# Kernel optimization log

Hardware: AMD Instinct MI355X
Metric: run time of the kernel (lower is better)

## Reference

```python
import jax, jax.numpy as jnp
import numpy as np

B, T_IN, T_OUT, N, C, H, K1 = 4, 12, 24, 5000, 32, 8, 17  # K1 = k+1 (self included)
SIGMA_RATIO = 2.0
BETA = 0.8  # Swish beta
W_THRESH = 1e-5


def setup_inputs() -> dict:
    key = jax.random.key(0)
    k1, k2, k3, k4, k5 = jax.random.split(key, 5)
    x = jax.random.normal(k1, (B, T_IN, N, C), jnp.float32)
    nearest_nodes = jax.random.randint(k2, (N, K1), 0, N)  # int indices; -1 allowed by module semantics
    nearest_dists = jax.random.uniform(k3, (N, K1), jnp.float32) * 100.0
    W_shrink = jax.random.normal(k4, (T_IN * H, T_OUT - T_IN), jnp.float32) / np.float32(np.sqrt(T_IN * H))
    b_shrink = jax.random.normal(k5, (T_OUT - T_IN,), jnp.float32) * 0.01
    return {"x": x, "nearest_nodes": nearest_nodes, "nearest_dists": nearest_dists,
            "W_shrink": W_shrink, "b_shrink": b_shrink}


def reference(x, nearest_nodes, nearest_dists, W_shrink, b_shrink):
    Bx, t, n, c = x.shape
    sigma = nearest_dists.max() / SIGMA_RATIO
    lam = jnp.arange(1, H + 1, dtype=jnp.float32) / H  # (H,)
    nd = nearest_dists.reshape(-1)                      # (N*K1,)
    nn = nearest_nodes.reshape(-1)                      # (N*K1,)
    # GCN weights: exp(-d^2 * lambda / sigma^2), zeroed for missing (-1) neighbors and tiny values
    w = jnp.exp(-(nd[:, None] ** 2) * lam / (sigma ** 2))  # (N*K1, H)
    w = jnp.where(nn[:, None] == -1, 0.0, w)
    w = jnp.where(w < W_THRESH, 0.0, w)
    # pad row so index -1 hits zeros (jax -1 wraps to last row, matching torch)
    pad_x = jnp.concatenate([x, jnp.zeros((Bx, t, 1, c), x.dtype)], axis=2)
    x_nb = pad_x[:, :, nn].reshape(Bx, t, n, K1, c)         # gathered neighbors (B,t,N,K1,C)
    w3 = w.reshape(n, K1, H)
    # fused gather-weight-sum over neighbor dim j -> (B,t,N,H,C)
    agg = jnp.einsum('btnjc,njh->btnhc', x_nb, w3)
    # (B,t,N,H,C) -> (B,N,C,t,H) -> (B,N,C,t*H)
    feat = agg.transpose(0, 2, 4, 1, 3).reshape(Bx, n, c, t * H)
    y = feat @ W_shrink + b_shrink                          # (B,N,C,T-t_in)
    y = y.transpose(0, 3, 1, 2)                             # (B,T-t_in,N,C)
    y = y * jax.nn.sigmoid(BETA * y)                        # Swish
    return jnp.concatenate([x, y], axis=1)                  # (B,T,N,C)
```

## Files before the change

kernel.cpp:

```cpp
#include <hip/hip_runtime.h>

#define BB     4
#define T_IN   12
#define T_OUT  24
#define NNODES 5000
#define CC     32
#define HH     8
#define K1     17
#define O_OUT  12
#define XSTRIDE (NNODES*CC)
#define TPU     (NNODES*16)

#define XB2_BN  192
#define XB2_B   (NNODES*XB2_BN)
#define JP      9
#define VJPD    36
#define VQD     (JP*VJPD)
#define VND     (4*VQD)
#define WJN     144

__global__ void max_reduce_kernel(const float* __restrict__ d, int n,
                                  unsigned* __restrict__ out) {
    float m = 0.0f;
    for (int i = blockIdx.x * blockDim.x + threadIdx.x; i < n;
         i += gridDim.x * blockDim.x)
        m = fmaxf(m, d[i]);
#pragma unroll
    for (int off = 32; off > 0; off >>= 1)
        m = fmaxf(m, __shfl_down(m, off, 64));
    if ((threadIdx.x & 63) == 0)
        atomicMax(out, __float_as_uint(m));
}

__device__ inline unsigned bf16rne(float f) {
    unsigned u = __float_as_uint(f);
    return (u + 0x7FFFu + ((u >> 16) & 1u)) >> 16;
}

__global__ void prep4_kernel(const float4* __restrict__ x,
                             float4* __restrict__ out,
                             uint4* __restrict__ xb2,
                             const int* __restrict__ nn,
                             const float* __restrict__ nd,
                             const unsigned* __restrict__ maxbits,
                             float* __restrict__ wjg) {
    const int gs = gridDim.x * blockDim.x;
    const int g0 = blockIdx.x * blockDim.x + threadIdx.x;

    const int totalA = BB * T_IN * NNODES;
    for (int i = g0; i < totalA; i += gs) {
        int bt = i / NNODES;
        int nd_ = i - bt * NNODES;
        int b  = bt / T_IN;
        int t  = bt - b * T_IN;
        const float4* xr = x + (size_t)i * 8;
        float4* orow = out + ((size_t)(b * T_OUT + t) * NNODES + nd_) * 8;
        uint4* xrow  = xb2 + ((size_t)(b * NNODES + nd_) * T_IN + t) * 4;
#pragma unroll
        for (int vq = 0; vq < 4; ++vq) {
            float4 v0 = xr[2 * vq], v1 = xr[2 * vq + 1];
            orow[2 * vq] = v0; orow[2 * vq + 1] = v1;
            uint4 pk;
            pk.x = bf16rne(v0.x) | (bf16rne(v0.y) << 16);
            pk.y = bf16rne(v0.z) | (bf16rne(v0.w) << 16);
            pk.z = bf16rne(v1.x) | (bf16rne(v1.y) << 16);
            pk.w = bf16rne(v1.z) | (bf16rne(v1.w) << 16);
            xrow[vq] = pk;
        }
    }

    float mx = __uint_as_float(*maxbits);
    float inv_s2 = 4.0f / (mx * mx);
    const int totalB = NNODES * WJN;
    for (int i = g0; i < totalB; i += gs) {
        int n = i / WJN;
        int r = i - n * WJN;
        int j = r >> 3, h = r & 7;
        float wv = 0.f;
        if (j < K1) {
            float dv = nd[n * K1 + j];
            float lam = (float)(h + 1) * 0.125f;
            wv = expf(-dv * dv * lam * inv_s2);
            if (nn[n * K1 + j] == -1 || wv < 1e-5f) wv = 0.0f;
        }
        wjg[i] = wv;
    }
}

struct VBlk { uint4 v[9]; };

__device__ __forceinline__ unsigned u4c(const uint4& u, int i) {
    switch (i) { case 0: return u.x; case 1: return u.y;
                 case 2: return u.z; default: return u.w; }
}

#define DOT2(ACC, XP, VP) \
    asm("v_dot2_f32_bf16 %0, %1, %2, %0" : "+v"(ACC) : "v"(XP), "v"(VP))

__launch_bounds__(256)
__global__ void gnn_main7_kernel(const unsigned* __restrict__ xb2,
                                 const float* __restrict__ wjg,
                                 const float* __restrict__ Wsh,
                                 const int* __restrict__ nn,
                                 const float* __restrict__ bsh,
                                 float* __restrict__ out) {
    __shared__ float pb2[2][24][65];
    __shared__ unsigned Vl[VND];
    __shared__ float bl[O_OUT];

    const int n    = blockIdx.x;
    const int tid  = threadIdx.x;
    const int q    = __builtin_amdgcn_readfirstlane(tid >> 6);
    const int lane = tid & 63;
    const int bb   = lane >> 4;
    const int c2   = lane & 15;

    if (tid < O_OUT) bl[tid] = bsh[tid];

    int nnv[18];
#pragma unroll
    for (int j = 0; j < K1; ++j) nnv[j] = max(nn[n * K1 + j], 0);
    nnv[17] = nnv[16];

    const unsigned* xlane = xb2 + bb * XB2_B + 48 * q + c2;

#define XLOADP(E0, E1, E2, O0, O1, O2, JPI) do {                             \
        const unsigned* xe_ = xlane + nnv[2 * (JPI)] * XB2_BN;               \
        const unsigned* xo_ = xlane + nnv[2 * (JPI) + 1] * XB2_BN;           \
        E0 = xe_[0]; E1 = xe_[16]; E2 = xe_[32];                             \
        O0 = xo_[0]; O1 = xo_[16]; O2 = xo_[32];                             \
    } while (0)

    unsigned e00, e01, e02, o00, o01, o02;
    unsigned e10, e11, e12, o10, o11, o12;
    unsigned e20, e21, e22, o20, o21, o22;

    XLOADP(e00, e01, e02, o00, o01, o02, 0);
    XLOADP(e10, e11, e12, o10, o11, o12, 1);

    {
        const int t = tid / 12;
        const int o = tid - t * 12;
        float Wcol[8];
        if (tid < 144) {
#pragma unroll
            for (int h = 0; h < 8; ++h) Wcol[h] = Wsh[(t * 8 + h) * 12 + o];
        }
        const float* wp = wjg + n * WJN;
        const int vi = (t / 3) * VQD + (t % 3) * 12 + o;
#pragma unroll
        for (int jp = 0; jp < JP; ++jp) {
            float wa[16];
#pragma unroll
            for (int h = 0; h < 16; ++h) wa[h] = wp[jp * 16 + h];
            if (tid < 144) {
                float v0 = 0.f, v1 = 0.f;
#pragma unroll
                for (int h = 0; h < 8; ++h) {
                    v0 = fmaf(wa[h],     Wcol[h], v0);
                    v1 = fmaf(wa[8 + h], Wcol[h], v1);
                }
                Vl[vi + jp * VJPD] = bf16rne(v0) | (bf16rne(v1) << 16);
            }
        }
    }

    float pf[24];
#pragma unroll
    for (int i = 0; i < 24; ++i) pf[i] = 0.f;

    __syncthreads();

#define VLOADP(DST, JPI) do {                                                \
        const uint4* vp_ = (const uint4*)&Vl[q * VQD + (JPI) * VJPD];        \
        _Pragma("unroll")                                                    \
        for (int i_ = 0; i_ < 9; ++i_) DST.v[i_] = vp_[i_];                  \
    } while (0)

#define COMPP(VV, E0, E1, E2, O0, O1, O2) do {                               \
        unsigned xe_[3] = {E0, E1, E2};                                      \
        unsigned xo_[3] = {O0, O1, O2};                                      \
        _Pragma("unroll")                                                    \
        for (int t_ = 0; t_ < 3; ++t_) {                                     \
            unsigned plo_ = __builtin_amdgcn_perm(xe_[t_], xo_[t_],          \
                                                  0x01000504u);              \
            unsigned phi_ = __builtin_amdgcn_perm(xe_[t_], xo_[t_],          \
                                                  0x03020706u);              \
            _Pragma("unroll")                                                \
            for (int o_ = 0; o_ < 12; ++o_) {                                \
                unsigned vp_ = u4c(VV.v[t_ * 3 + (o_ >> 2)], o_ & 3);        \
                DOT2(pf[o_],      plo_, vp_);                                \
                DOT2(pf[12 + o_], phi_, vp_);                                \
            }                                                                \
        }                                                                    \
    } while (0)

    VBlk va, vb;
    VLOADP(va, 0);
    VLOADP(vb, 1);
    XLOADP(e20, e21, e22, o20, o21, o22, 2);
    COMPP(va, e00, e01, e02, o00, o01, o02);
    VLOADP(va, 2);
    XLOADP(e00, e01, e02, o00, o01, o02, 3);
    COMPP(vb, e10, e11, e12, o10, o11, o12);
    VLOADP(vb, 3);
    XLOADP(e10, e11, e12, o10, o11, o12, 4);
    COMPP(va, e20, e21, e22, o20, o21, o22);
    VLOADP(va, 4);
    XLOADP(e20, e21, e22, o20, o21, o22, 5);
    COMPP(vb, e00, e01, e02, o00, o01, o02);
    VLOADP(vb, 5);
    XLOADP(e00, e01, e02, o00, o01, o02, 6);
    COMPP(va, e10, e11, e12, o10, o11, o12);
    VLOADP(va, 6);
    XLOADP(e10, e11, e12, o10, o11, o12, 7);
    COMPP(vb, e20, e21, e22, o20, o21, o22);
    VLOADP(vb, 7);
    XLOADP(e20, e21, e22, o20, o21, o22, 8);
    COMPP(va, e00, e01, e02, o00, o01, o02);
    VLOADP(va, 8);
    COMPP(vb, e10, e11, e12, o10, o11, o12);
    COMPP(va, e20, e21, e22, o20, o21, o22);

#undef VLOADP
#undef XLOADP
#undef COMPP

    if (q >= 2) {
#pragma unroll
        for (int i = 0; i < 24; ++i) pb2[q - 2][i][lane] = pf[i];
    }
    __syncthreads();
    if (q < 2) {
#pragma unroll
        for (int i = 0; i < 24; ++i) pf[i] += pb2[q][i][lane];
    }
    if (q == 1) {
#pragma unroll
        for (int i = 0; i < 24; ++i) pb2[1][i][lane] = pf[i];
    }
    __syncthreads();
    if (q == 0) {
        float* ob = out + ((size_t)(bb * T_OUT + T_IN) * NNODES + n) * CC + 2 * c2;
#pragma unroll
        for (int o = 0; o < O_OUT; ++o) {
            float v0 = pf[o]      + pb2[1][o][lane]      + bl[o];
            float v1 = pf[12 + o] + pb2[1][12 + o][lane] + bl[o];
            float s0 = v0 / (1.f + expf(-0.8f * v0));
            float s1 = v1 / (1.f + expf(-0.8f * v1));
            *(float2*)(ob + (size_t)o * XSTRIDE) = make_float2(s0, s1);
        }
    }
}

template <int PACK>
__global__ void prep_kernel(const float4* __restrict__ x,
                            float4* __restrict__ out,
                            uint2* __restrict__ xb) {
    const int PLANE4 = NNODES * CC / 4;
    const int total  = BB * T_IN * PLANE4;
    for (int i = blockIdx.x * blockDim.x + threadIdx.x; i < total;
         i += gridDim.x * blockDim.x) {
        int bt = i / PLANE4;
        int qq = i - bt * PLANE4;
        int b  = bt / T_IN;
        int t  = bt - b * T_IN;
        float4 v = x[i];
        out[((size_t)(b * T_OUT + t)) * PLANE4 + qq] = v;
        if (PACK) {
            uint2 pk;
            pk.x = bf16rne(v.x) | (bf16rne(v.y) << 16);
            pk.y = bf16rne(v.z) | (bf16rne(v.w) << 16);
            xb[i] = pk;
        }
    }
}

template <int USEBF>
__launch_bounds__(256)
__global__ void gnn_main_kernel(const float* __restrict__ x,
                                const unsigned* __restrict__ xbu,
                                const int* __restrict__ nn,
                                const float* __restrict__ nd,
                                const float* __restrict__ Wsh,
                                const float* __restrict__ bsh,
                                const unsigned* __restrict__ maxbits,
                                float* __restrict__ out) {
    __shared__ float wl[K1][HH];
    __shared__ float Wl[96][O_OUT];
    __shared__ float bl_s[O_OUT];
    __shared__ int   nnl[K1];

    const int n   = blockIdx.x;
    const int tid = threadIdx.x;
    const int rg  = tid >> 4;
    const int c2  = tid & 15;
    const int b   = rg >> 2;
    const int q   = rg & 3;

    for (int i = tid; i < 288; i += 256)
        ((float4*)Wl)[i] = ((const float4*)Wsh)[i];
    if (tid < O_OUT) bl_s[tid] = bsh[tid];
    if (tid < K1 * HH) {
        int j = tid >> 3, h = tid & 7;
        int v = nn[n * K1 + j];
        float dv = nd[n * K1 + j];
        float mx = __uint_as_float(*maxbits);
        float inv_s2 = 4.0f / (mx * mx);
        float lam = (float)(h + 1) * 0.125f;
        float wv = expf(-dv * dv * lam * inv_s2);
        if (v == -1 || wv < 1e-5f) wv = 0.0f;
        wl[j][h] = wv;
    }
    if (tid < K1) nnl[tid] = max(nn[n * K1 + tid], 0);
    __syncthreads();

    float acc[3][2][8];
#pragma unroll
    for (int k = 0; k < 3; ++k)
#pragma unroll
        for (int cc = 0; cc < 2; ++cc)
#pragma unroll
            for (int h = 0; h < 8; ++h) acc[k][cc][h] = 0.f;

    if (USEBF) {
        const unsigned* xbase = xbu + (b * T_IN + 3 * q) * TPU + c2;
        unsigned ua0, ua1, ua2, ub0, ub1, ub2;
#define LOADB(u0, u1, u2, J) do {                                            \
        int idx_ = __builtin_amdgcn_readfirstlane(nnl[(J)]);                 \
        const unsigned* bp_ = xbase + idx_ * 16;                             \
        u0 = bp_[0]; u1 = bp_[TPU]; u2 = bp_[2 * TPU];                       \
    } while (0)
#define COMPB(u0, u1, u2, J) do {                                            \
        float4 wA_ = *(const float4*)&wl[(J)][0];                            \
        float4 wB_ = *(const float4*)&wl[(J)][4];                            \
        float wv_[8] = {wA_.x, wA_.y, wA_.z, wA_.w,                          \
                        wB_.x, wB_.y, wB_.z, wB_.w};                         \
        float xl_[3] = {__uint_as_float(u0 << 16),                           \
                        __uint_as_float(u1 << 16),                           \
                        __uint_as_float(u2 << 16)};                          \
        float xh_[3] = {__uint_as_float(u0 & 0xffff0000u),                   \
                        __uint_as_float(u1 & 0xffff0000u),                   \
                        __uint_as_float(u2 & 0xffff0000u)};                  \
        _Pragma("unroll")                                                    \
        for (int k_ = 0; k_ < 3; ++k_)                                       \
            _Pragma("unroll")                                                \
            for (int h_ = 0; h_ < 8; ++h_) {                                 \
                acc[k_][0][h_] = fmaf(wv_[h_], xl_[k_], acc[k_][0][h_]);     \
                acc[k_][1][h_] = fmaf(wv_[h_], xh_[k_], acc[k_][1][h_]);     \
            }                                                                \
    } while (0)
        LOADB(ua0, ua1, ua2, 0);
#pragma unroll 1
        for (int jj = 0; jj < 8; ++jj) {
            LOADB(ub0, ub1, ub2, 2 * jj + 1);
            COMPB(ua0, ua1, ua2, 2 * jj);
            LOADB(ua0, ua1, ua2, 2 * jj + 2);
            COMPB(ub0, ub1, ub2, 2 * jj + 1);
        }
        COMPB(ua0, ua1, ua2, 16);
#undef LOADB
#undef COMPB
    } else {
        const float* xbase = x + (b * T_IN + 3 * q) * XSTRIDE + 2 * c2;
        float2 xa0, xa1, xa2, xb0, xb1, xb2;
#define LOADJ(v0, v1, v2, J) do {                                            \
        int idx_ = __builtin_amdgcn_readfirstlane(nnl[(J)]);                 \
        const float* bp_ = xbase + idx_ * CC;                                \
        v0 = *(const float2*)(bp_);                                          \
        v1 = *(const float2*)(bp_ + XSTRIDE);                                \
        v2 = *(const float2*)(bp_ + 2 * XSTRIDE);                            \
    } while (0)
#define COMPJ(v0, v1, v2, J) do {                                            \
        float4 wA_ = *(const float4*)&wl[(J)][0];                            \
        float4 wB_ = *(const float4*)&wl[(J)][4];                            \
        float wv_[8] = {wA_.x, wA_.y, wA_.z, wA_.w,                          \
                        wB_.x, wB_.y, wB_.z, wB_.w};                         \
        float xv_[3][2] = {{v0.x, v0.y}, {v1.x, v1.y}, {v2.x, v2.y}};        \
        _Pragma("unroll")                                                    \
        for (int k_ = 0; k_ < 3; ++k_)                                       \
            _Pragma("unroll")                                                \
            for (int cc_ = 0; cc_ < 2; ++cc_)                                \
                _Pragma("unroll")                                            \
                for (int h_ = 0; h_ < 8; ++h_)                               \
                    acc[k_][cc_][h_] =                                       \
                        fmaf(wv_[h_], xv_[k_][cc_], acc[k_][cc_][h_]);       \
    } while (0)
        LOADJ(xa0, xa1, xa2, 0);
#pragma unroll 1
        for (int jj = 0; jj < 8; ++jj) {
            LOADJ(xb0, xb1, xb2, 2 * jj + 1);
            COMPJ(xa0, xa1, xa2, 2 * jj);
            LOADJ(xa0, xa1, xa2, 2 * jj + 2);
            COMPJ(xb0, xb1, xb2, 2 * jj + 1);
        }
        COMPJ(xa0, xa1, xa2, 16);
#undef LOADJ
#undef COMPJ
    }

    float p[2][O_OUT];
#pragma unroll
    for (int o = 0; o < O_OUT; ++o) { p[0][o] = 0.f; p[1][o] = 0.f; }
#pragma unroll
    for (int k = 0; k < 3; ++k) {
#pragma unroll
        for (int h = 0; h < 8; ++h) {
            int row = (3 * q + k) * 8 + h;
            const float4* wr = (const float4*)&Wl[row][0];
            float4 w0 = wr[0], w1 = wr[1], w2 = wr[2];
            float wrow[12] = {w0.x, w0.y, w0.z, w0.w,
                              w1.x, w1.y, w1.z, w1.w,
                              w2.x, w2.y, w2.z, w2.w};
            float a0 = acc[k][0][h], a1 = acc[k][1][h];
#pragma unroll
            for (int o = 0; o < O_OUT; ++o) {
                p[0][o] = fmaf(a0, wrow[o], p[0][o]);
                p[1][o] = fmaf(a1, wrow[o], p[1][o]);
            }
        }
    }
#pragma unroll
    for (int cc = 0; cc < 2; ++cc)
#pragma unroll
        for (int o = 0; o < O_OUT; ++o) {
            float v = p[cc][o];
            v += __shfl_xor(v, 16, 64);
            v += __shfl_xor(v, 32, 64);
            p[cc][o] = v;
        }
    if (q == 0) {
        float* ob = out + ((size_t)(b * T_OUT + T_IN) * NNODES + n) * CC + 2 * c2;
#pragma unroll
        for (int o = 0; o < O_OUT; ++o) {
            float v0 = p[0][o] + bl_s[o];
            float v1 = p[1][o] + bl_s[o];
            float s0 = v0 / (1.f + expf(-0.8f * v0));
            float s1 = v1 / (1.f + expf(-0.8f * v1));
            *(float2*)(ob + (size_t)o * XSTRIDE) = make_float2(s0, s1);
        }
    }
}

extern "C" void kernel_launch(void* const* d_in, const int* in_sizes, int n_in,
                              void* d_out, int out_size, void* d_ws, size_t ws_size,
                              hipStream_t stream) {
    const float* x   = (const float*)d_in[0];
    const int*   nn  = (const int*)d_in[1];
    const float* nd  = (const float*)d_in[2];
    const float* Wsh = (const float*)d_in[3];
    const float* bsh = (const float*)d_in[4];
    float* out = (float*)d_out;

    unsigned* maxbits = (unsigned*)d_ws;
    hipMemsetAsync(d_ws, 0, sizeof(unsigned), stream);
    max_reduce_kernel<<<128, 256, 0, stream>>>(nd, NNODES * K1, maxbits);

    const size_t wjg_off = 1024;
    const size_t wjg_sz  = (size_t)NNODES * WJN * 4;
    const size_t xb2_off = wjg_off + wjg_sz;
    const size_t xb2_sz  = (size_t)BB * NNODES * T_IN * 16 * 4;
    const size_t need2   = xb2_off + xb2_sz;

    if (ws_size >= need2) {
        float* wjg = (float*)((char*)d_ws + wjg_off);
        uint4* xb2 = (uint4*)((char*)d_ws + xb2_off);

        prep4_kernel<<<2048, 256, 0, stream>>>(
            (const float4*)x, (float4*)out, xb2, nn, nd, maxbits, wjg);
        gnn_main7_kernel<<<NNODES, 256, 0, stream>>>(
            (const unsigned*)xb2, wjg, Wsh, nn, bsh, out);
    } else {
        unsigned* xbu = (unsigned*)((char*)d_ws + 256);
        const size_t need1 = 256 + (size_t)BB * T_IN * NNODES * CC * 2;
        if (ws_size >= need1) {
            prep_kernel<1><<<2048, 256, 0, stream>>>((const float4*)x,
                                                     (float4*)out, (uint2*)xbu);
            gnn_main_kernel<1><<<NNODES, 256, 0, stream>>>(x, xbu, nn, nd, Wsh,
                                                           bsh, maxbits, out);
        } else {
            prep_kernel<0><<<2048, 256, 0, stream>>>((const float4*)x,
                                                     (float4*)out, (uint2*)xbu);
            gnn_main_kernel<0><<<NNODES, 256, 0, stream>>>(x, xbu, nn, nd, Wsh,
                                                           bsh, maxbits, out);
        }
    }
}
```

Measured before the change: 86.42 us.

## Fold max-reduce into prep kernel and compute GCN weights inside main kernel

Drops the separate max-reduction launch by having the prep kernel compute the distance max with an atomic. The per-node Gaussian weights are no longer written to a global workspace buffer. Each main-kernel block now computes its 144 weights in shared memory before building its bf16 V table. This saves one kernel launch and a global write/read of the weight table, at the cost of an extra block barrier and exp work inside the main kernel.

Measured after the change: 90.61 us. 1.05x slower.

```diff
diff --git a/kernel.cpp b/kernel.cpp
--- a/kernel.cpp
+++ b/kernel.cpp
@@ -17,7 +17,6 @@
 #define VJPD    36
 #define VQD     (JP*VJPD)
 #define VND     (4*VQD)
-#define WJN     144
 
 __global__ void max_reduce_kernel(const float* __restrict__ d, int n,
                                   unsigned* __restrict__ out) {
@@ -37,15 +36,23 @@
     return (u + 0x7FFFu + ((u >> 16) & 1u)) >> 16;
 }
 
-__global__ void prep4_kernel(const float4* __restrict__ x,
+__global__ void prep5_kernel(const float4* __restrict__ x,
                              float4* __restrict__ out,
                              uint4* __restrict__ xb2,
-                             const int* __restrict__ nn,
                              const float* __restrict__ nd,
-                             const unsigned* __restrict__ maxbits,
-                             float* __restrict__ wjg) {
+                             unsigned* __restrict__ maxbits) {
     const int gs = gridDim.x * blockDim.x;
     const int g0 = blockIdx.x * blockDim.x + threadIdx.x;
+
+    {
+        float m = 0.0f;
+        for (int i = g0; i < NNODES * K1; i += gs) m = fmaxf(m, nd[i]);
+#pragma unroll
+        for (int off = 32; off > 0; off >>= 1)
+            m = fmaxf(m, __shfl_down(m, off, 64));
+        if ((threadIdx.x & 63) == 0 && m > 0.0f)
+            atomicMax(maxbits, __float_as_uint(m));
+    }
 
     const int totalA = BB * T_IN * NNODES;
     for (int i = g0; i < totalA; i += gs) {
@@ -68,23 +75,6 @@
             xrow[vq] = pk;
         }
     }
-
-    float mx = __uint_as_float(*maxbits);
-    float inv_s2 = 4.0f / (mx * mx);
-    const int totalB = NNODES * WJN;
-    for (int i = g0; i < totalB; i += gs) {
-        int n = i / WJN;
-        int r = i - n * WJN;
-        int j = r >> 3, h = r & 7;
-        float wv = 0.f;
-        if (j < K1) {
-            float dv = nd[n * K1 + j];
-            float lam = (float)(h + 1) * 0.125f;
-            wv = expf(-dv * dv * lam * inv_s2);
-            if (nn[n * K1 + j] == -1 || wv < 1e-5f) wv = 0.0f;
-        }
-        wjg[i] = wv;
-    }
 }
 
 struct VBlk { uint4 v[9]; };
@@ -98,14 +88,16 @@
     asm("v_dot2_f32_bf16 %0, %1, %2, %0" : "+v"(ACC) : "v"(XP), "v"(VP))
 
 __launch_bounds__(256)
-__global__ void gnn_main7_kernel(const unsigned* __restrict__ xb2,
-                                 const float* __restrict__ wjg,
+__global__ void gnn_main9_kernel(const unsigned* __restrict__ xb2,
+                                 const float* __restrict__ nd,
                                  const float* __restrict__ Wsh,
                                  const int* __restrict__ nn,
                                  const float* __restrict__ bsh,
+                                 const unsigned* __restrict__ maxbits,
                                  float* __restrict__ out) {
     __shared__ float pb2[2][24][65];
     __shared__ unsigned Vl[VND];
+    __shared__ float wjl[144];
     __shared__ float bl[O_OUT];
 
     const int n    = blockIdx.x;
@@ -138,30 +130,43 @@
     XLOADP(e00, e01, e02, o00, o01, o02, 0);
     XLOADP(e10, e11, e12, o10, o11, o12, 1);
 
-    {
-        const int t = tid / 12;
-        const int o = tid - t * 12;
-        float Wcol[8];
-        if (tid < 144) {
-#pragma unroll
-            for (int h = 0; h < 8; ++h) Wcol[h] = Wsh[(t * 8 + h) * 12 + o];
-        }
-        const float* wp = wjg + n * WJN;
-        const int vi = (t / 3) * VQD + (t % 3) * 12 + o;
+    const int t14 = tid / 12;
+    const int o14 = tid - t14 * 12;
+    float Wcol[8];
+    if (tid < 144) {
+#pragma unroll
+        for (int h = 0; h < 8; ++h) Wcol[h] = Wsh[(t14 * 8 + h) * 12 + o14];
+        int j = tid >> 3, h = tid & 7;
+        float wv = 0.f;
+        if (j < K1) {
+            float mx = __uint_as_float(*maxbits);
+            float inv_s2 = 4.0f / (mx * mx);
+            float dv = nd[n * K1 + j];
+            float lam = (float)(h + 1) * 0.125f;
+            wv = expf(-dv * dv * lam * inv_s2);
+            if (nn[n * K1 + j] == -1 || wv < 1e-5f) wv = 0.0f;
+        }
+        wjl[tid] = wv;
+    }
+    __syncthreads();
+
+    if (tid < 144) {
+        const int vi = (t14 / 3) * VQD + (t14 % 3) * 12 + o14;
 #pragma unroll
         for (int jp = 0; jp < JP; ++jp) {
-            float wa[16];
-#pragma unroll
-            for (int h = 0; h < 16; ++h) wa[h] = wp[jp * 16 + h];
-            if (tid < 144) {
-                float v0 = 0.f, v1 = 0.f;
-#pragma unroll
-                for (int h = 0; h < 8; ++h) {
-                    v0 = fmaf(wa[h],     Wcol[h], v0);
-                    v1 = fmaf(wa[8 + h], Wcol[h], v1);
-                }
-                Vl[vi + jp * VJPD] = bf16rne(v0) | (bf16rne(v1) << 16);
+            float4 a0 = *(const float4*)&wjl[jp * 16];
+            float4 a1 = *(const float4*)&wjl[jp * 16 + 4];
+            float4 b0 = *(const float4*)&wjl[jp * 16 + 8];
+            float4 b1 = *(const float4*)&wjl[jp * 16 + 12];
+            float wa[8] = {a0.x, a0.y, a0.z, a0.w, a1.x, a1.y, a1.z, a1.w};
+            float wb[8] = {b0.x, b0.y, b0.z, b0.w, b1.x, b1.y, b1.z, b1.w};
+            float v0 = 0.f, v1 = 0.f;
+#pragma unroll
+            for (int h = 0; h < 8; ++h) {
+                v0 = fmaf(wa[h], Wcol[h], v0);
+                v1 = fmaf(wb[h], Wcol[h], v1);
             }
+            Vl[vi + jp * VJPD] = bf16rne(v0) | (bf16rne(v1) << 16);
         }
     }
 
@@ -454,23 +459,20 @@
 
     unsigned* maxbits = (unsigned*)d_ws;
     hipMemsetAsync(d_ws, 0, sizeof(unsigned), stream);
-    max_reduce_kernel<<<128, 256, 0, stream>>>(nd, NNODES * K1, maxbits);
-
-    const size_t wjg_off = 1024;
-    const size_t wjg_sz  = (size_t)NNODES * WJN * 4;
-    const size_t xb2_off = wjg_off + wjg_sz;
+
+    const size_t xb2_off = 1024;
     const size_t xb2_sz  = (size_t)BB * NNODES * T_IN * 16 * 4;
     const size_t need2   = xb2_off + xb2_sz;
 
     if (ws_size >= need2) {
-        float* wjg = (float*)((char*)d_ws + wjg_off);
         uint4* xb2 = (uint4*)((char*)d_ws + xb2_off);
 
-        prep4_kernel<<<2048, 256, 0, stream>>>(
-            (const float4*)x, (float4*)out, xb2, nn, nd, maxbits, wjg);
-        gnn_main7_kernel<<<NNODES, 256, 0, stream>>>(
-            (const unsigned*)xb2, wjg, Wsh, nn, bsh, out);
+        prep5_kernel<<<2048, 256, 0, stream>>>(
+            (const float4*)x, (float4*)out, xb2, nd, maxbits);
+        gnn_main9_kernel<<<NNODES, 256, 0, stream>>>(
+            (const unsigned*)xb2, nd, Wsh, nn, bsh, maxbits, out);
     } else {
+        max_reduce_kernel<<<128, 256, 0, stream>>>(nd, NNODES * K1, maxbits);
         unsigned* xbu = (unsigned*)((char*)d_ws + 256);
         const size_t need1 = 256 + (size_t)BB * T_IN * NNODES * CC * 2;
         if (ws_size >= need1) {
```
